# Performance work log

Hardware: AMD Instinct MI355X
Metric: run time of the kernel (lower is better)

Reference implementation:

```python
import jax, jax.numpy as jnp
import numpy as np

N, L, K, D = 131072, 8, 1024, 1024


def setup_inputs() -> dict:
    key = jax.random.key(0)
    k1, k2 = jax.random.split(key)
    x = jax.random.randint(k1, (N, L), 0, K, dtype=jnp.int32)
    weight = jax.random.normal(k2, (L, K, D), dtype=jnp.float32)
    return {"x": x, "weight": weight}


def reference(x, weight):
    # Original: one-hot(x) -> [N, L, K]; einsum('l k d, n l k -> n d', w, oh)
    # == sum over levels of a direct embedding gather:
    #   out[n] = sum_l weight[l, x[n, l], :]
    L_ = weight.shape[0]
    gathered = weight[jnp.arange(L_)[None, :], x, :]  # [N, L, D]
    return gathered.sum(axis=1)  # [N, D]
```

## Files before the change

kernel.cpp:

```cpp
#include <hip/hip_runtime.h>


#define N_ROWS 131072
#define L_DIM 8
#define K_DIM 1024
#define D_DIM 1024

#define NXCD 8
#define RPB 128
#define CR 16
#define NCH (RPB / CR)
#define GRID_CHUNKS (N_ROWS / RPB)
#define W_ELEMS (L_DIM * K_DIM * D_DIM)

typedef float        f32x4 __attribute__((ext_vector_type(4)));
typedef unsigned int u32x2 __attribute__((ext_vector_type(2)));

__device__ __forceinline__ unsigned short f2bf_rne(float f) {
    unsigned u = __float_as_uint(f);
    unsigned r = u + 0x7fffu + ((u >> 16) & 1u);
    return (unsigned short)(r >> 16);
}
__device__ __forceinline__ float bflo(unsigned u) { return __uint_as_float(u << 16); }
__device__ __forceinline__ float bfhi(unsigned u) { return __uint_as_float(u & 0xffff0000u); }

__device__ __forceinline__ void load_lds16(const void* g, void* l) {
    __builtin_amdgcn_global_load_lds(
        (const __attribute__((address_space(1))) void*)g,
        (__attribute__((address_space(3))) void*)l,
        16, 0, 0);
}

__global__ __launch_bounds__(256) void convert_w_bf16(
    const float* __restrict__ w, unsigned short* __restrict__ wb)
{
    const int i = blockIdx.x * 256 + threadIdx.x;
    const f32x4 v = __builtin_nontemporal_load(
        reinterpret_cast<const f32x4*>(w) + i);
    ushort4 o;
    o.x = f2bf_rne(v.x); o.y = f2bf_rne(v.y);
    o.z = f2bf_rne(v.z); o.w = f2bf_rne(v.w);
    reinterpret_cast<ushort4*>(wb)[i] = o;
}

__global__ __launch_bounds__(256) void gather_sum_dma(
    const int* __restrict__ x,
    const unsigned short* __restrict__ wb,
    float* __restrict__ out)
{
    __shared__ int sxi[RPB * L_DIM];
    __shared__ __align__(1024) char buf[2][CR * L_DIM * 256];

    const int slice = blockIdx.x & (NXCD - 1);
    const int chunk = blockIdx.x >> 3;
    const int t     = threadIdx.x;
    const int n0    = chunk * RPB;

    if (t < RPB * L_DIM / 4)
        reinterpret_cast<int4*>(sxi)[t] =
            reinterpret_cast<const int4*>(x + (size_t)n0 * L_DIM)[t];
    __syncthreads();

    const int w_id = t >> 6;
    const int lam  = t & 63;
    const int grp  = lam >> 4;
    const int sub  = lam & 15;
    const int half = (t >> 5) & 1;
    const int lane = t & 31;

    const unsigned colb = (unsigned)slice << 8;
    const char* __restrict__ wbytes = (const char*)wb;

    #pragma unroll
    for (int i = 0; i < 8; ++i) {
        const int j = w_id * 8 + i;
        const int g = 4 * j + grp;
        const int l = g & 7;
        const int k = sxi[g];
        const unsigned off = (((unsigned)((l << 10) + k)) << 11) + colb
                           + (unsigned)sub * 16u;
        load_lds16(wbytes + off, &buf[0][j * 1024]);
    }
    __syncthreads();

    #pragma unroll
    for (int c = 0; c < NCH; ++c) {
        if (c + 1 < NCH) {
            #pragma unroll
            for (int i = 0; i < 8; ++i) {
                const int j = w_id * 8 + i;
                const int g = 4 * j + grp;
                const int l = g & 7;
                const int k = sxi[(c + 1) * 128 + g];
                const unsigned off = (((unsigned)((l << 10) + k)) << 11) + colb
                                   + (unsigned)sub * 16u;
                load_lds16(wbytes + off, &buf[(c + 1) & 1][j * 1024]);
            }
        }

        const char* __restrict__ rb = buf[c & 1];
        #pragma unroll
        for (int s = 0; s < 2; ++s) {
            const int r = w_id * 4 + s * 2 + half;
            u32x2 v[L_DIM];
            #pragma unroll
            for (int l = 0; l < L_DIM; ++l)
                v[l] = *reinterpret_cast<const u32x2*>(
                    rb + (r * 8 + l) * 256 + lane * 8);

            f32x4 acc = (f32x4)(0.f);
            #pragma unroll
            for (int l = 0; l < L_DIM; ++l) {
                acc.x += bflo(v[l][0]); acc.y += bfhi(v[l][0]);
                acc.z += bflo(v[l][1]); acc.w += bfhi(v[l][1]);
            }

            const int n = n0 + c * CR + r;
            __builtin_nontemporal_store(acc,
                reinterpret_cast<f32x4*>(
                    out + (size_t)n * D_DIM + slice * 128 + lane * 4));
        }

        __syncthreads();
    }
}

__global__ __launch_bounds__(256) void gather_sum_f32(
    const int* __restrict__ x,
    const float* __restrict__ w,
    float* __restrict__ out)
{
    __shared__ int sxi[RPB * L_DIM];
    const int slice = blockIdx.x & (NXCD - 1);
    const int chunk = blockIdx.x >> 3;
    const int t     = threadIdx.x;
    const int n0    = chunk * RPB;

    if (t < RPB * L_DIM / 4)
        reinterpret_cast<int4*>(sxi)[t] =
            reinterpret_cast<const int4*>(x + (size_t)n0 * L_DIM)[t];
    __syncthreads();

    const int rg   = t >> 5;
    const int lane = t & 31;
    const int col  = slice * 128 + lane * 4;
    const float* __restrict__ wbase = w + col;

    #pragma unroll
    for (int i = 0; i < 8; ++i) {
        const int rA = rg + 16 * i;
        const int rB = rA + 8;
        const int* xA = sxi + rA * L_DIM;
        const int* xB = sxi + rB * L_DIM;
        f32x4 vA[L_DIM], vB[L_DIM];
        #pragma unroll
        for (int l = 0; l < L_DIM; ++l)
            vA[l] = *reinterpret_cast<const f32x4*>(
                wbase + (size_t)(l * K_DIM + xA[l]) * D_DIM);
        #pragma unroll
        for (int l = 0; l < L_DIM; ++l)
            vB[l] = *reinterpret_cast<const f32x4*>(
                wbase + (size_t)(l * K_DIM + xB[l]) * D_DIM);
        f32x4 accA = ((vA[0] + vA[1]) + (vA[2] + vA[3]))
                   + ((vA[4] + vA[5]) + (vA[6] + vA[7]));
        f32x4 accB = ((vB[0] + vB[1]) + (vB[2] + vB[3]))
                   + ((vB[4] + vB[5]) + (vB[6] + vB[7]));
        __builtin_nontemporal_store(accA,
            reinterpret_cast<f32x4*>(out + (size_t)(n0 + rA) * D_DIM + col));
        __builtin_nontemporal_store(accB,
            reinterpret_cast<f32x4*>(out + (size_t)(n0 + rB) * D_DIM + col));
    }
}

extern "C" void kernel_launch(void* const* d_in, const int* in_sizes, int n_in,
                              void* d_out, int out_size, void* d_ws, size_t ws_size,
                              hipStream_t stream)
{
    const int*   x = (const int*)d_in[0];
    const float* w = (const float*)d_in[1];
    float* out = (float*)d_out;

    if (ws_size >= (size_t)W_ELEMS * 2) {
        unsigned short* wb = (unsigned short*)d_ws;
        convert_w_bf16<<<W_ELEMS / 4 / 256, 256, 0, stream>>>(w, wb);
        gather_sum_dma<<<GRID_CHUNKS * NXCD, 256, 0, stream>>>(x, wb, out);
    } else {
        gather_sum_f32<<<GRID_CHUNKS * NXCD, 256, 0, stream>>>(x, w, out);
    }
}
```

Before: 152.6 us.

## Pipeline gather with 3-buffer vmcnt waits and swizzled bf16 weight layout

Replaces the double-buffered, barrier-synchronised gather with a three-buffer pipeline of prefetch depth two over smaller 8-row chunks. Each wave waits with explicit s_waitcnt vmcnt counts instead of block-wide __syncthreads, which is possible because each wave consumes only the rows it loaded itself. The bf16 conversion kernel now rotates the 128-column slices per (level, key) row, and the gather reads with the matching rotation, so different slices hit spread-out addresses. This gives more loads in flight and removes barriers, but it depends on hand-computed wait counts (including the outstanding stores) being exactly right.

```diff
diff --git a/kernel.cpp b/kernel.cpp
--- a/kernel.cpp
+++ b/kernel.cpp
@@ -8,8 +8,11 @@
 
 #define NXCD 8
 #define RPB 128
-#define CR 16
+#define CR 8
 #define NCH (RPB / CR)
+#define PFD 2
+#define NBUF (PFD + 1)
+#define CHB (CR * L_DIM * 256)
 #define GRID_CHUNKS (N_ROWS / RPB)
 #define W_ELEMS (L_DIM * K_DIM * D_DIM)
 
@@ -29,6 +32,18 @@
         (const __attribute__((address_space(1))) void*)g,
         (__attribute__((address_space(3))) void*)l,
         16, 0, 0);
+}
+
+template <int N>
+__device__ __forceinline__ void vm_wait() {
+    asm volatile("s_waitcnt vmcnt(%0)" :: "n"(N) : "memory");
+    __builtin_amdgcn_sched_barrier(0);
+}
+
+constexpr int waitn(int c) {
+    int nl = (c + PFD <= NCH - 1) ? PFD : (NCH - 1 - c);
+    int ns = (c < PFD) ? c : PFD;
+    return 4 * nl + ns;
 }
 
 __global__ __launch_bounds__(256) void convert_w_bf16(
@@ -40,25 +55,31 @@
     ushort4 o;
     o.x = f2bf_rne(v.x); o.y = f2bf_rne(v.y);
     o.z = f2bf_rne(v.z); o.w = f2bf_rne(v.w);
-    reinterpret_cast<ushort4*>(wb)[i] = o;
-}
-
-__global__ __launch_bounds__(256) void gather_sum_dma(
+
+    const int rk = i >> 8;
+    const int c0 = (i & 255) * 4;
+    const int l  = rk >> 10;
+    const int k  = rk & 1023;
+    const int r  = (l + k) & 7;
+    const int c2 = (c0 + r * 128) & 1023;
+    *reinterpret_cast<ushort4*>(wb + ((size_t)rk << 10) + c2) = o;
+}
+
+__global__ __launch_bounds__(256) void gather_sum_pipe(
     const int* __restrict__ x,
     const unsigned short* __restrict__ wb,
     float* __restrict__ out)
 {
     __shared__ int sxi[RPB * L_DIM];
-    __shared__ __align__(1024) char buf[2][CR * L_DIM * 256];
+    __shared__ __align__(1024) char buf[NBUF * CHB];
 
     const int slice = blockIdx.x & (NXCD - 1);
     const int chunk = blockIdx.x >> 3;
     const int t     = threadIdx.x;
     const int n0    = chunk * RPB;
 
-    if (t < RPB * L_DIM / 4)
-        reinterpret_cast<int4*>(sxi)[t] =
-            reinterpret_cast<const int4*>(x + (size_t)n0 * L_DIM)[t];
+    reinterpret_cast<int4*>(sxi)[t] =
+        reinterpret_cast<const int4*>(x + (size_t)n0 * L_DIM)[t];
     __syncthreads();
 
     const int w_id = t >> 6;
@@ -68,61 +89,58 @@
     const int half = (t >> 5) & 1;
     const int lane = t & 31;
 
-    const unsigned colb = (unsigned)slice << 8;
     const char* __restrict__ wbytes = (const char*)wb;
 
-    #pragma unroll
-    for (int i = 0; i < 8; ++i) {
-        const int j = w_id * 8 + i;
-        const int g = 4 * j + grp;
-        const int l = g & 7;
-        const int k = sxi[g];
-        const unsigned off = (((unsigned)((l << 10) + k)) << 11) + colb
-                           + (unsigned)sub * 16u;
-        load_lds16(wbytes + off, &buf[0][j * 1024]);
+    auto issue = [&](int c) {
+        char* __restrict__ db = buf + (c % NBUF) * CHB;
+        #pragma unroll
+        for (int i = 0; i < 4; ++i) {
+            const int j = w_id * 4 + i;
+            const int g = 4 * j + grp;
+            const int l = g & 7;
+            const int k = sxi[c * 64 + g];
+            const int r = (slice + l + k) & 7;
+            const unsigned off =
+                ((unsigned)((l << 10) + k) << 11) + ((unsigned)r << 8)
+                + (unsigned)sub * 16u;
+            load_lds16(wbytes + off, db + j * 1024);
+        }
+    };
+
+    auto consume = [&](int c) {
+        const char* __restrict__ rb = buf + (c % NBUF) * CHB;
+        const int g0 = w_id * 16 + half * 8;
+        u32x2 v[L_DIM];
+        #pragma unroll
+        for (int l = 0; l < L_DIM; ++l)
+            v[l] = *reinterpret_cast<const u32x2*>(
+                rb + (g0 + l) * 256 + lane * 8);
+        f32x4 acc = (f32x4)(0.f);
+        #pragma unroll
+        for (int l = 0; l < L_DIM; ++l) {
+            acc.x += bflo(v[l][0]); acc.y += bfhi(v[l][0]);
+            acc.z += bflo(v[l][1]); acc.w += bfhi(v[l][1]);
+        }
+        const int n = n0 + c * CR + 2 * w_id + half;
+        __builtin_nontemporal_store(acc,
+            reinterpret_cast<f32x4*>(
+                out + (size_t)n * D_DIM + slice * 128 + lane * 4));
+    };
+
+    issue(0);
+    issue(1);
+
+#define STEP(c)                                   \
+    {                                             \
+        if ((c) + PFD < NCH) issue((c) + PFD);    \
+        vm_wait<waitn(c)>();                      \
+        consume(c);                               \
     }
-    __syncthreads();
-
-    #pragma unroll
-    for (int c = 0; c < NCH; ++c) {
-        if (c + 1 < NCH) {
-            #pragma unroll
-            for (int i = 0; i < 8; ++i) {
-                const int j = w_id * 8 + i;
-                const int g = 4 * j + grp;
-                const int l = g & 7;
-                const int k = sxi[(c + 1) * 128 + g];
-                const unsigned off = (((unsigned)((l << 10) + k)) << 11) + colb
-                                   + (unsigned)sub * 16u;
-                load_lds16(wbytes + off, &buf[(c + 1) & 1][j * 1024]);
-            }
-        }
-
-        const char* __restrict__ rb = buf[c & 1];
-        #pragma unroll
-        for (int s = 0; s < 2; ++s) {
-            const int r = w_id * 4 + s * 2 + half;
-            u32x2 v[L_DIM];
-            #pragma unroll
-            for (int l = 0; l < L_DIM; ++l)
-                v[l] = *reinterpret_cast<const u32x2*>(
-                    rb + (r * 8 + l) * 256 + lane * 8);
-
-            f32x4 acc = (f32x4)(0.f);
-            #pragma unroll
-            for (int l = 0; l < L_DIM; ++l) {
-                acc.x += bflo(v[l][0]); acc.y += bfhi(v[l][0]);
-                acc.z += bflo(v[l][1]); acc.w += bfhi(v[l][1]);
-            }
-
-            const int n = n0 + c * CR + r;
-            __builtin_nontemporal_store(acc,
-                reinterpret_cast<f32x4*>(
-                    out + (size_t)n * D_DIM + slice * 128 + lane * 4));
-        }
-
-        __syncthreads();
-    }
+    STEP(0)  STEP(1)  STEP(2)  STEP(3)
+    STEP(4)  STEP(5)  STEP(6)  STEP(7)
+    STEP(8)  STEP(9)  STEP(10) STEP(11)
+    STEP(12) STEP(13) STEP(14) STEP(15)
+#undef STEP
 }
 
 __global__ __launch_bounds__(256) void gather_sum_f32(
@@ -136,9 +154,8 @@
     const int t     = threadIdx.x;
     const int n0    = chunk * RPB;
 
-    if (t < RPB * L_DIM / 4)
-        reinterpret_cast<int4*>(sxi)[t] =
-            reinterpret_cast<const int4*>(x + (size_t)n0 * L_DIM)[t];
+    reinterpret_cast<int4*>(sxi)[t] =
+        reinterpret_cast<const int4*>(x + (size_t)n0 * L_DIM)[t];
     __syncthreads();
 
     const int rg   = t >> 5;
@@ -183,7 +200,7 @@
     if (ws_size >= (size_t)W_ELEMS * 2) {
         unsigned short* wb = (unsigned short*)d_ws;
         convert_w_bf16<<<W_ELEMS / 4 / 256, 256, 0, stream>>>(w, wb);
-        gather_sum_dma<<<GRID_CHUNKS * NXCD, 256, 0, stream>>>(x, wb, out);
+        gather_sum_pipe<<<GRID_CHUNKS * NXCD, 256, 0, stream>>>(x, wb, out);
     } else {
         gather_sum_f32<<<GRID_CHUNKS * NXCD, 256, 0, stream>>>(x, w, out);
     }
```

Result: faster. 145.5 us, median of 2 (-4.6%).
